# Optimization experiments

Measured on AMD Instinct MI355X. Metric: run time of the kernel, lower is better.

## Reference

```python
import jax, jax.numpy as jnp
import numpy as np

NUM_CATEGORIES = 64
INPUT_DIM = 256
HIDDEN_DIM = 256
N = 4096  # number of samples (each with its own category)
M = 16    # rows per sample


def setup_inputs() -> dict:
    key = jax.random.key(0)
    k_x, k_cat, k_W = jax.random.split(key, 3)
    x = jax.random.normal(k_x, (N, M, INPUT_DIM), dtype=jnp.float32)
    cat_ids = jax.random.randint(k_cat, (N,), 0, NUM_CATEGORIES, dtype=jnp.int64)
    W = 0.02 * jax.random.normal(k_W, (NUM_CATEGORIES, INPUT_DIM, HIDDEN_DIM), dtype=jnp.float32)
    b = jnp.zeros((NUM_CATEGORIES, HIDDEN_DIM), dtype=jnp.float32)
    return {"x": x, "cat_ids": cat_ids, "W": W, "b": b}


def reference(x, cat_ids, W, b):
    # Gather per-sample weights/biases, then batched matmul + bias add.
    selected_W = W[cat_ids]              # [N, input_dim, hidden_dim]
    selected_b = b[cat_ids]              # [N, hidden_dim]
    out = jnp.einsum('nmi,nih->nmh', x, selected_W) + selected_b[:, None, :]
    return out
```

## Files before the change

kernel.cpp:

```cpp
#include <hip/hip_runtime.h>
#include <hip/hip_bf16.h>
#include <stdint.h>

#define N_SAMPLES 4096
#define M_ROWS 16
#define K_DIM 256
#define H_DIM 256
#define N_CATS 64
#define SPB 4
#define MAX_PADDED (N_SAMPLES + N_CATS * (SPB - 1))
#define NGROUP (MAX_PADDED / SPB)
#define GPX (NGROUP / 8)

typedef _Float16 half8 __attribute__((ext_vector_type(8)));
typedef _Float16 half4 __attribute__((ext_vector_type(4)));
typedef float floatx4 __attribute__((ext_vector_type(4)));

#define WT_BYTES ((size_t)N_CATS * K_DIM * H_DIM * 2)
#define GCAT_OFF WT_BYTES
#define ORD_OFF  (WT_BYTES + 4288)
#define WS_NEED  (ORD_OFF + (size_t)MAX_PADDED * 4)

__global__ __launch_bounds__(256)
void prep_combined(const float* __restrict__ W, _Float16* __restrict__ Wt,
                   const int* __restrict__ cat, int* __restrict__ ord,
                   int* __restrict__ gcat) {
  const int tid = threadIdx.x;
  if (blockIdx.x < 1024) {
    __shared__ _Float16 t[64][72];
    const int bid = blockIdx.x;
    const int c  = bid >> 4;
    const int kb = (bid >> 2) & 3;
    const int hb = bid & 3;
    const int r  = tid >> 2;
    const int cg = (tid & 3) * 16;
    const float* src = W + ((size_t)c << 16) + (size_t)(kb * 64 + r) * 256 + hb * 64 + cg;
#pragma unroll
    for (int j = 0; j < 16; j += 4) {
      float4 v = *(const float4*)(src + j);
      t[r][cg + j + 0] = (_Float16)v.x;
      t[r][cg + j + 1] = (_Float16)v.y;
      t[r][cg + j + 2] = (_Float16)v.z;
      t[r][cg + j + 3] = (_Float16)v.w;
    }
    __syncthreads();
    _Float16* dst = Wt + ((size_t)c << 16) + (size_t)(hb * 64 + r) * 256 + kb * 64 + cg;
    half8 o0, o1;
#pragma unroll
    for (int j = 0; j < 8; j++) o0[j] = t[cg + j][r];
#pragma unroll
    for (int j = 0; j < 8; j++) o1[j] = t[cg + 8 + j][r];
    *(half8*)(dst) = o0;
    *(half8*)(dst + 8) = o1;
  } else {
    __shared__ int hist[N_CATS];
    __shared__ int poffs[N_CATS];
    __shared__ int curs[N_CATS];
    if (tid < N_CATS) hist[tid] = 0;
    for (int i = tid; i < MAX_PADDED; i += 256) ord[i] = -1;
    for (int i = tid; i < NGROUP; i += 256) gcat[i] = 0;
    __syncthreads();
    for (int i = tid; i < N_SAMPLES; i += 256) atomicAdd(&hist[cat[i]], 1);
    __syncthreads();
    if (tid == 0) {
      int run = 0;
      for (int c = 0; c < N_CATS; c++) {
        poffs[c] = run;
        run += ((hist[c] + SPB - 1) / SPB) * SPB;
      }
    }
    if (tid < N_CATS) curs[tid] = 0;
    __syncthreads();
    if (tid < N_CATS) {
      const int c = tid;
      const int g0 = poffs[c] >> 2;
      const int ng = (hist[c] + SPB - 1) >> 2;
      for (int g = 0; g < ng; g++) gcat[g0 + g] = c;
    }
    for (int i = tid; i < N_SAMPLES; i += 256) {
      int c = cat[i];
      int p = poffs[c] + atomicAdd(&curs[c], 1);
      ord[p] = i;
    }
  }
}

__global__ __launch_bounds__(512, 6)
void gemm_kernel(const float* __restrict__ x, const float* __restrict__ bias,
                 const _Float16* __restrict__ Wt, const int* __restrict__ ord,
                 const int* __restrict__ gcat, float* __restrict__ out) {
  __shared__ __align__(16) _Float16 sA[64 * 256];

  const int tid = threadIdx.x;
  const int B = blockIdx.x;
  const int xcd = B & 7;
  const int group = xcd * GPX + (B >> 3);

  const int cat = gcat[group];
  const int4 sm = *(const int4*)(ord + group * 4);
  if (sm.x < 0) return;

  const int wid  = tid >> 6;
  const int lane = tid & 63;
  const int l15  = lane & 15;
  const int quad = lane >> 4;

  const _Float16* wbase = Wt + ((size_t)cat << 16);
  const _Float16* bptr0 = wbase + (size_t)(wid * 32 + 0 * 16 + l15) * K_DIM + quad * 8;
  const _Float16* bptr1 = wbase + (size_t)(wid * 32 + 1 * 16 + l15) * K_DIM + quad * 8;

  half8 bf[3][2];
#pragma unroll
  for (int kt = 0; kt < 2; kt++) {
    bf[kt][0] = *(const half8*)(bptr0 + kt * 32);
    bf[kt][1] = *(const half8*)(bptr1 + kt * 32);
  }
  __builtin_amdgcn_sched_barrier(0);

  const float* b0 = (sm.x >= 0) ? x + ((size_t)sm.x << 12) : nullptr;
  const float* b1 = (sm.y >= 0) ? x + ((size_t)sm.y << 12) : nullptr;
  const float* b2 = (sm.z >= 0) ? x + ((size_t)sm.z << 12) : nullptr;
  const float* b3 = (sm.w >= 0) ? x + ((size_t)sm.w << 12) : nullptr;
  const int wcol = (lane * 4) ^ (wid << 3);
#pragma unroll
  for (int i = 0; i < 8; i++) {
    const float* bs = ((i >> 1) == 0) ? b0 : ((i >> 1) == 1) ? b1 : ((i >> 1) == 2) ? b2 : b3;
    const int row = i * 8 + wid;
    _Float16* adst = sA + row * 256 + wcol;
    if (bs) {
      float4 v = *(const float4*)(bs + (size_t)(((i & 1) * 8 + wid) * 256) + lane * 4);
      half4 h;
      h[0] = (_Float16)v.x; h[1] = (_Float16)v.y;
      h[2] = (_Float16)v.z; h[3] = (_Float16)v.w;
      *(half4*)adst = h;
    } else {
      half4 h;
#pragma unroll
      for (int e = 0; e < 4; e++) h[e] = (_Float16)0.0f;
      *(half4*)adst = h;
    }
  }

  floatx4 acc[4][2];
#pragma unroll
  for (int i = 0; i < 4; i++)
#pragma unroll
    for (int j = 0; j < 2; j++)
#pragma unroll
      for (int e = 0; e < 4; e++) acc[i][j][e] = 0.0f;

  __syncthreads();

  const int swz = (l15 & 7) << 3;
#pragma unroll
  for (int kt = 0; kt < 8; kt++) {
    if (kt < 6) {
      const int nx = (kt + 2) % 3;
      bf[nx][0] = *(const half8*)(bptr0 + (kt + 2) * 32);
      bf[nx][1] = *(const half8*)(bptr1 + (kt + 2) * 32);
    }
    const int cur = kt % 3;
    half8 af[4];
#pragma unroll
    for (int mt = 0; mt < 4; mt++)
      af[mt] = *(const half8*)&sA[(mt * 16 + l15) * 256 + ((kt * 32 + quad * 8) ^ swz)];
#pragma unroll
    for (int mt = 0; mt < 4; mt++) {
      acc[mt][0] = __builtin_amdgcn_mfma_f32_16x16x32_f16(af[mt], bf[cur][0], acc[mt][0], 0, 0, 0);
      acc[mt][1] = __builtin_amdgcn_mfma_f32_16x16x32_f16(af[mt], bf[cur][1], acc[mt][1], 0, 0, 0);
    }
  }

  float bv[2];
#pragma unroll
  for (int nt = 0; nt < 2; nt++)
    bv[nt] = bias[cat * H_DIM + wid * 32 + nt * 16 + l15];
  const int srow[4] = {sm.x, sm.y, sm.z, sm.w};
#pragma unroll
  for (int mt = 0; mt < 4; mt++) {
    const int s = srow[mt];
    if (s < 0) continue;
    float* obase = out + ((size_t)s << 12);
#pragma unroll
    for (int nt = 0; nt < 2; nt++) {
      const int col = wid * 32 + nt * 16 + l15;
#pragma unroll
      for (int rr = 0; rr < 4; rr++) {
        const int row = quad * 4 + rr;
        obase[(size_t)row * H_DIM + col] = acc[mt][nt][rr] + bv[nt];
      }
    }
  }
}

__global__ __launch_bounds__(256)
void naive_kernel(const float* __restrict__ x, const int* __restrict__ cat,
                  const float* __restrict__ W, const float* __restrict__ bias,
                  float* __restrict__ out) {
  __shared__ float sx[16 * 256];
  const int n = blockIdx.x;
  const int tid = threadIdx.x;
  const int c = cat[n];
  const float* xs = x + (size_t)n * 16 * 256;
  for (int i = tid; i < 16 * 256; i += 256) sx[i] = xs[i];
  __syncthreads();
  const float* Wc = W + ((size_t)c << 16);
  float accv[16];
  float bv = bias[c * 256 + tid];
#pragma unroll
  for (int m = 0; m < 16; m++) accv[m] = bv;
  for (int k = 0; k < 256; k++) {
    float w = Wc[(size_t)k * 256 + tid];
#pragma unroll
    for (int m = 0; m < 16; m++) accv[m] += sx[m * 256 + k] * w;
  }
#pragma unroll
  for (int m = 0; m < 16; m++) out[((size_t)n * 16 + m) * 256 + tid] = accv[m];
}

extern "C" void kernel_launch(void* const* d_in, const int* in_sizes, int n_in,
                              void* d_out, int out_size, void* d_ws, size_t ws_size,
                              hipStream_t stream) {
  const float* x    = (const float*)d_in[0];
  const int*   cat  = (const int*)d_in[1];
  const float* W    = (const float*)d_in[2];
  const float* bias = (const float*)d_in[3];
  float* out = (float*)d_out;

  if (ws_size < WS_NEED) {
    naive_kernel<<<N_SAMPLES, 256, 0, stream>>>(x, cat, W, bias, out);
    return;
  }

  char* ws = (char*)d_ws;
  _Float16* Wt = (_Float16*)ws;
  int* gcat = (int*)(ws + GCAT_OFF);
  int* ord  = (int*)(ws + ORD_OFF);

  prep_combined<<<1025, 256, 0, stream>>>(W, Wt, cat, ord, gcat);
  gemm_kernel<<<NGROUP, 512, 0, stream>>>(x, bias, Wt, ord, gcat, out);
}
```

Measured before the change: 166.6 us.

## Stage x via direct global-to-LDS loads in fp32 and convert at fragment read

The A-tile of x is now copied straight from global memory into LDS as fp32 using global_load_lds, skipping the register round trip and the fp16 conversion in the load phase. Conversion to fp16 moves into the MFMA loop at fragment-read time, using a re-derived XOR swizzle for fp32. Padded sample slots now read sample 0's data instead of writing zeros, and their outputs are still skipped. W fragments are fully prefetched into an 8-deep register buffer, the bias load is hoisted, and outputs use nontemporal stores. The trade is doubled LDS footprint (64 KB per block), lower occupancy (launch bound 4 instead of 6), and more register use.

After: 168.2 us. About the same (+1.0%).

```diff
diff --git a/kernel.cpp b/kernel.cpp
--- a/kernel.cpp
+++ b/kernel.cpp
@@ -15,6 +15,11 @@
 typedef _Float16 half8 __attribute__((ext_vector_type(8)));
 typedef _Float16 half4 __attribute__((ext_vector_type(4)));
 typedef float floatx4 __attribute__((ext_vector_type(4)));
+
+#define GLOAD_LDS(g, l)                                          \
+  __builtin_amdgcn_global_load_lds(                              \
+      (const __attribute__((address_space(1))) void*)(g),        \
+      (__attribute__((address_space(3))) void*)(l), 16, 0, 0)
 
 #define WT_BYTES ((size_t)N_CATS * K_DIM * H_DIM * 2)
 #define GCAT_OFF WT_BYTES
@@ -85,11 +90,11 @@
   }
 }
 
-__global__ __launch_bounds__(512, 6)
+__global__ __launch_bounds__(512, 4)
 void gemm_kernel(const float* __restrict__ x, const float* __restrict__ bias,
                  const _Float16* __restrict__ Wt, const int* __restrict__ ord,
                  const int* __restrict__ gcat, float* __restrict__ out) {
-  __shared__ __align__(16) _Float16 sA[64 * 256];
+  __shared__ __align__(16) float sA[64 * 256];
 
   const int tid = threadIdx.x;
   const int B = blockIdx.x;
@@ -105,41 +110,27 @@
   const int l15  = lane & 15;
   const int quad = lane >> 4;
 
-  const _Float16* wbase = Wt + ((size_t)cat << 16);
-  const _Float16* bptr0 = wbase + (size_t)(wid * 32 + 0 * 16 + l15) * K_DIM + quad * 8;
-  const _Float16* bptr1 = wbase + (size_t)(wid * 32 + 1 * 16 + l15) * K_DIM + quad * 8;
-
-  half8 bf[3][2];
-#pragma unroll
-  for (int kt = 0; kt < 2; kt++) {
-    bf[kt][0] = *(const half8*)(bptr0 + kt * 32);
-    bf[kt][1] = *(const half8*)(bptr1 + kt * 32);
-  }
-  __builtin_amdgcn_sched_barrier(0);
-
-  const float* b0 = (sm.x >= 0) ? x + ((size_t)sm.x << 12) : nullptr;
-  const float* b1 = (sm.y >= 0) ? x + ((size_t)sm.y << 12) : nullptr;
-  const float* b2 = (sm.z >= 0) ? x + ((size_t)sm.z << 12) : nullptr;
-  const float* b3 = (sm.w >= 0) ? x + ((size_t)sm.w << 12) : nullptr;
-  const int wcol = (lane * 4) ^ (wid << 3);
+  const int s0 = sm.x;
+  const int s1 = sm.y < 0 ? sm.x : sm.y;
+  const int s2 = sm.z < 0 ? sm.x : sm.z;
+  const int s3 = sm.w < 0 ? sm.x : sm.w;
+  const int lx = (lane ^ wid) << 2;
 #pragma unroll
   for (int i = 0; i < 8; i++) {
-    const float* bs = ((i >> 1) == 0) ? b0 : ((i >> 1) == 1) ? b1 : ((i >> 1) == 2) ? b2 : b3;
-    const int row = i * 8 + wid;
-    _Float16* adst = sA + row * 256 + wcol;
-    if (bs) {
-      float4 v = *(const float4*)(bs + (size_t)(((i & 1) * 8 + wid) * 256) + lane * 4);
-      half4 h;
-      h[0] = (_Float16)v.x; h[1] = (_Float16)v.y;
-      h[2] = (_Float16)v.z; h[3] = (_Float16)v.w;
-      *(half4*)adst = h;
-    } else {
-      half4 h;
-#pragma unroll
-      for (int e = 0; e < 4; e++) h[e] = (_Float16)0.0f;
-      *(half4*)adst = h;
-    }
-  }
+    const int smp = ((i >> 1) == 0) ? s0 : ((i >> 1) == 1) ? s1 : ((i >> 1) == 2) ? s2 : s3;
+    const float* gp = x + ((size_t)smp << 12) + (size_t)((i & 1) * 8 + wid) * 256 + lx;
+    GLOAD_LDS(gp, sA + (i * 8 + wid) * 256);
+  }
+
+  const _Float16* wb = Wt + ((size_t)cat << 16) + (size_t)(wid * 32 + l15) * K_DIM + quad * 8;
+  half8 bf[8][2];
+#pragma unroll
+  for (int kt = 0; kt < 4; kt++) {
+    bf[kt][0] = *(const half8*)(wb + kt * 32);
+    bf[kt][1] = *(const half8*)(wb + 16 * K_DIM + kt * 32);
+  }
+  const float bv0 = bias[cat * H_DIM + wid * 32 + l15];
+  const float bv1 = bias[cat * H_DIM + wid * 32 + 16 + l15];
 
   floatx4 acc[4][2];
 #pragma unroll
@@ -151,30 +142,31 @@
 
   __syncthreads();
 
-  const int swz = (l15 & 7) << 3;
+  const int swz = (l15 & 7) << 2;
 #pragma unroll
   for (int kt = 0; kt < 8; kt++) {
-    if (kt < 6) {
-      const int nx = (kt + 2) % 3;
-      bf[nx][0] = *(const half8*)(bptr0 + (kt + 2) * 32);
-      bf[nx][1] = *(const half8*)(bptr1 + (kt + 2) * 32);
-    }
-    const int cur = kt % 3;
+    if (kt < 4) {
+      bf[kt + 4][0] = *(const half8*)(wb + (kt + 4) * 32);
+      bf[kt + 4][1] = *(const half8*)(wb + 16 * K_DIM + (kt + 4) * 32);
+    }
     half8 af[4];
 #pragma unroll
-    for (int mt = 0; mt < 4; mt++)
-      af[mt] = *(const half8*)&sA[(mt * 16 + l15) * 256 + ((kt * 32 + quad * 8) ^ swz)];
-#pragma unroll
     for (int mt = 0; mt < 4; mt++) {
-      acc[mt][0] = __builtin_amdgcn_mfma_f32_16x16x32_f16(af[mt], bf[cur][0], acc[mt][0], 0, 0, 0);
-      acc[mt][1] = __builtin_amdgcn_mfma_f32_16x16x32_f16(af[mt], bf[cur][1], acc[mt][1], 0, 0, 0);
-    }
-  }
-
-  float bv[2];
-#pragma unroll
-  for (int nt = 0; nt < 2; nt++)
-    bv[nt] = bias[cat * H_DIM + wid * 32 + nt * 16 + l15];
+      const float* ap = sA + (size_t)(mt * 16 + l15) * 256;
+      float4 f0 = *(const float4*)(ap + ((kt * 32 + quad * 8 + 0) ^ swz));
+      float4 f1 = *(const float4*)(ap + ((kt * 32 + quad * 8 + 4) ^ swz));
+      af[mt][0] = (_Float16)f0.x; af[mt][1] = (_Float16)f0.y;
+      af[mt][2] = (_Float16)f0.z; af[mt][3] = (_Float16)f0.w;
+      af[mt][4] = (_Float16)f1.x; af[mt][5] = (_Float16)f1.y;
+      af[mt][6] = (_Float16)f1.z; af[mt][7] = (_Float16)f1.w;
+    }
+#pragma unroll
+    for (int mt = 0; mt < 4; mt++) {
+      acc[mt][0] = __builtin_amdgcn_mfma_f32_16x16x32_f16(af[mt], bf[kt][0], acc[mt][0], 0, 0, 0);
+      acc[mt][1] = __builtin_amdgcn_mfma_f32_16x16x32_f16(af[mt], bf[kt][1], acc[mt][1], 0, 0, 0);
+    }
+  }
+
   const int srow[4] = {sm.x, sm.y, sm.z, sm.w};
 #pragma unroll
   for (int mt = 0; mt < 4; mt++) {
@@ -184,10 +176,11 @@
 #pragma unroll
     for (int nt = 0; nt < 2; nt++) {
       const int col = wid * 32 + nt * 16 + l15;
+      const float bv = nt ? bv1 : bv0;
 #pragma unroll
       for (int rr = 0; rr < 4; rr++) {
         const int row = quad * 4 + rr;
-        obase[(size_t)row * H_DIM + col] = acc[mt][nt][rr] + bv[nt];
+        __builtin_nontemporal_store(acc[mt][nt][rr] + bv, obase + (size_t)row * H_DIM + col);
       }
     }
   }
```
